# Optimization experiments

Measured on AMD Instinct MI355X. Metric: run time of the kernel, lower is better.

The kernel has to match this reference:

```python
import jax, jax.numpy as jnp
import numpy as np

B, N, D_IN, D_H, D_OUT = 32, 512, 512, 512, 512


def _xavier(key, fan_in, fan_out):
    bound = np.sqrt(6.0 / (fan_in + fan_out))
    return jax.random.uniform(key, (fan_in, fan_out), jnp.float32, -bound, bound)


def setup_inputs() -> dict:
    key = jax.random.key(0)
    ks = jax.random.split(key, 8)
    batch_graph = jax.random.normal(ks[0], (B, N, D_IN), jnp.float32)
    adj = jax.random.uniform(ks[1], (B, N, N), jnp.float32)  # per-graph adjacency blocks
    W0 = _xavier(ks[2], D_IN, D_H)
    b0 = jnp.zeros((D_H,), jnp.float32)
    W1 = _xavier(ks[3], D_H, D_H)
    b1 = jnp.zeros((D_H,), jnp.float32)
    W2 = _xavier(ks[4], D_H, D_OUT)
    b2 = jnp.zeros((D_OUT,), jnp.float32)
    return {"batch_graph": batch_graph, "adj": adj,
            "W0": W0, "b0": b0, "W1": W1, "b1": b1, "W2": W2, "b2": b2}


def _gcn_layer(h, adj, W, b):
    # GraphConvolution: adj @ (h @ W) + b, batched per graph.
    # Equivalent to big_adj @ (big_graph @ W) since big_adj is block-diagonal.
    support = jnp.einsum('bnd,de->bne', h, W)
    return jnp.einsum('bnm,bme->bne', adj, support) + b


def reference(batch_graph, adj, W0, b0, W1, b1, W2, b2):
    # dropout is identity at inference time
    h = jax.nn.relu(_gcn_layer(batch_graph, adj, W0, b0))
    h = jax.nn.relu(_gcn_layer(h, adj, W1, b1))
    h = _gcn_layer(h, adj, W2, b2)  # no activation on final layer
    return h  # [B, N, D_OUT] == torch.stack(big_graph.split(N))
```

## Files before the change

### kernel.cpp

```cpp
#include <hip/hip_runtime.h>
#include <stdint.h>

typedef __bf16 bf16x8 __attribute__((ext_vector_type(8)));
typedef float f32x4 __attribute__((ext_vector_type(4)));
typedef unsigned short u16x4 __attribute__((ext_vector_type(4)));

static __device__ __forceinline__ unsigned short f2bf(float f) {
    union { float f; unsigned u; } v; v.f = f;
    unsigned r = (v.u + 0x7FFFu + ((v.u >> 16) & 1u)) >> 16;
    return (unsigned short)r;
}

__global__ void prep_kernel(const float* __restrict__ X,
                            const float* __restrict__ adj,
                            const float* __restrict__ W0,
                            const float* __restrict__ W1,
                            const float* __restrict__ W2,
                            unsigned short* __restrict__ bufH,
                            unsigned short* __restrict__ adjB,
                            unsigned short* __restrict__ Wt) {
    const int bid = blockIdx.x;
    const int t = threadIdx.x;
    if (bid < 16384) {
        const float* src = (bid < 8192) ? X : adj;
        unsigned short* dst = (bid < 8192) ? bufH : adjB;
        const int i = (bid & 8191) * 256 + t;
        f32x4 v = ((const f32x4*)src)[i];
        u16x4 o;
        o.x = f2bf(v.x); o.y = f2bf(v.y); o.z = f2bf(v.z); o.w = f2bf(v.w);
        ((u16x4*)dst)[i] = o;
    } else {
        const int wb = bid - 16384;
        const int z = wb >> 8;
        const int tile = wb & 255;
        const float* W = (z == 0) ? W0 : (z == 1) ? W1 : W2;
        unsigned short* out = Wt + (size_t)z * (512 * 512);
        __shared__ float tileS[32][33];
        const int bx = (tile & 15) * 32, by = (tile >> 4) * 32;
        const int tx = t & 31, ty = t >> 5;
        #pragma unroll
        for (int r = 0; r < 32; r += 8)
            tileS[ty + r][tx] = W[(size_t)(by + ty + r) * 512 + (bx + tx)];
        __syncthreads();
        #pragma unroll
        for (int r = 0; r < 32; r += 8)
            out[(size_t)(bx + ty + r) * 512 + (by + tx)] = f2bf(tileS[tx][ty + r]);
    }
}

template<int LDA, int LDB, int LDO, bool BIAS, bool RELU, bool ADJ, typename OT>
__global__ __launch_bounds__(256, 2)
void gemm_abT_ct(const unsigned short* __restrict__ A,
                 const unsigned short* __restrict__ B,
                 OT* __restrict__ out, const float* __restrict__ bias,
                 long batchA, long batchB, long batchO) {
    __shared__ char SMEM[65536];
    unsigned short (*As)[8192] = (unsigned short (*)[8192])SMEM;
    unsigned short (*Bs)[8192] = (unsigned short (*)[8192])(SMEM + 32768);

    const int tid  = threadIdx.x;
    const int lane = tid & 63;
    const int wave = tid >> 6;
    const int quad = lane >> 4;
    const int l16  = lane & 15;
    const int wm   = wave & 1;
    const int wn   = wave >> 1;

    const int L = blockIdx.x;
    const int x = L & 7;
    const int j = L >> 3;
    int m0, n0;
    long z;
    if constexpr (ADJ) {
        z = x + 8 * (j >> 4);
        const int t4 = j & 15;
        m0 = (t4 & 3) * 128;
        n0 = (t4 >> 2) * 128;
    } else {
        z = 0;
        m0 = (x * 16 + (j >> 2)) * 128;
        n0 = (j & 3) * 128;
    }
    A   += (size_t)z * batchA;
    B   += (size_t)z * batchB;
    out += (size_t)z * batchO;

    const int trow8 = tid >> 3;
    const int tpos8 = (tid & 7) ^ (trow8 & 7);
    const unsigned short* aG = A + (size_t)(m0 + trow8) * LDA + tpos8 * 8;
    const unsigned short* bG = B + (size_t)(n0 + trow8) * LDB + tpos8 * 8;

    f32x4 acc[4][4];
    #pragma unroll
    for (int i = 0; i < 4; ++i)
        #pragma unroll
        for (int j2 = 0; j2 < 4; ++j2) {
            f32x4 zz = {0.f, 0.f, 0.f, 0.f};
            acc[i][j2] = zz;
        }

#define STAGE(buf, ko)                                                         \
    do {                                                                       \
        char* aL = (char*)(As[buf]) + tid * 16;                                \
        char* bL = (char*)(Bs[buf]) + tid * 16;                                \
        _Pragma("unroll")                                                      \
        for (int r = 0; r < 4; ++r)                                            \
            __builtin_amdgcn_global_load_lds(                                  \
                (__attribute__((address_space(1))) void*)(uintptr_t)(aG + (size_t)(r * 32) * LDA + (ko)), \
                (__attribute__((address_space(3))) void*)(aL + r * 4096), 16, 0, 0); \
        _Pragma("unroll")                                                      \
        for (int r = 0; r < 4; ++r)                                            \
            __builtin_amdgcn_global_load_lds(                                  \
                (__attribute__((address_space(1))) void*)(uintptr_t)(bG + (size_t)(r * 32) * LDB + (ko)), \
                (__attribute__((address_space(3))) void*)(bL + r * 4096), 16, 0, 0); \
    } while (0)

#define COMPUTE(buf)                                                           \
    do {                                                                       \
        _Pragma("unroll")                                                      \
        for (int ks = 0; ks < 2; ++ks) {                                       \
            bf16x8 af[4], bfr[4];                                              \
            _Pragma("unroll")                                                  \
            for (int i = 0; i < 4; ++i) {                                      \
                const int row = wm * 64 + i * 16 + l16;                        \
                const int idx = row * 8 + ((ks * 4 + quad) ^ (row & 7));       \
                af[i] = *(const bf16x8*)((const char*)(As[buf]) + idx * 16);   \
            }                                                                  \
            _Pragma("unroll")                                                  \
            for (int j2 = 0; j2 < 4; ++j2) {                                   \
                const int row = wn * 64 + j2 * 16 + l16;                       \
                const int idx = row * 8 + ((ks * 4 + quad) ^ (row & 7));       \
                bfr[j2] = *(const bf16x8*)((const char*)(Bs[buf]) + idx * 16); \
            }                                                                  \
            _Pragma("unroll")                                                  \
            for (int i = 0; i < 4; ++i)                                        \
                _Pragma("unroll")                                              \
                for (int j2 = 0; j2 < 4; ++j2)                                 \
                    acc[i][j2] = __builtin_amdgcn_mfma_f32_16x16x32_bf16(af[i], bfr[j2], acc[i][j2], 0, 0, 0); \
        }                                                                      \
    } while (0)

    STAGE(0, 0);
    STAGE(1, 64);

    #pragma unroll 1
    for (int kp = 0; kp < 4; ++kp) {
        const int ko = kp * 128;
        asm volatile("s_waitcnt vmcnt(8)" ::: "memory");
        __builtin_amdgcn_s_barrier();
        __builtin_amdgcn_s_setprio(1);
        COMPUTE(0);
        __builtin_amdgcn_s_setprio(0);
        asm volatile("s_waitcnt lgkmcnt(0)" ::: "memory");
        __builtin_amdgcn_sched_barrier(0);
        __builtin_amdgcn_s_barrier();
        if (kp < 3) STAGE(0, ko + 128);
        if (kp < 3) asm volatile("s_waitcnt vmcnt(8)" ::: "memory");
        else        asm volatile("s_waitcnt vmcnt(0)" ::: "memory");
        __builtin_amdgcn_s_barrier();
        __builtin_amdgcn_s_setprio(1);
        COMPUTE(1);
        __builtin_amdgcn_s_setprio(0);
        asm volatile("s_waitcnt lgkmcnt(0)" ::: "memory");
        __builtin_amdgcn_sched_barrier(0);
        __builtin_amdgcn_s_barrier();
        if (kp < 3) STAGE(1, ko + 192);
    }
#undef STAGE
#undef COMPUTE

    if constexpr (sizeof(OT) == 2) {
        unsigned short* T = (unsigned short*)SMEM;
        #pragma unroll
        for (int i = 0; i < 4; ++i) {
            const int mloc = wm * 64 + i * 16 + quad * 4;
            const int mb = m0 + mloc;
            f32x4 bb = {0.f, 0.f, 0.f, 0.f};
            if constexpr (BIAS) bb = *(const f32x4*)(bias + mb);
            const int ch  = mloc >> 3;
            const int sub = (mloc & 7) * 2;
            #pragma unroll
            for (int j2 = 0; j2 < 4; ++j2) {
                const int nloc = wn * 64 + j2 * 16 + l16;
                f32x4 v = acc[i][j2];
                if constexpr (BIAS) v += bb;
                if constexpr (RELU) {
                    v.x = v.x > 0.f ? v.x : 0.f;
                    v.y = v.y > 0.f ? v.y : 0.f;
                    v.z = v.z > 0.f ? v.z : 0.f;
                    v.w = v.w > 0.f ? v.w : 0.f;
                }
                u16x4 o;
                o.x = f2bf(v.x); o.y = f2bf(v.y); o.z = f2bf(v.z); o.w = f2bf(v.w);
                *(u16x4*)((char*)T + nloc * 256 + ((ch ^ (nloc & 7)) << 4) + sub) = o;
            }
        }
        __syncthreads();
        #pragma unroll
        for (int it = 0; it < 8; ++it) {
            const int n  = (tid >> 4) + 16 * it;
            const int cc = tid & 15;
            f32x4 d = *(const f32x4*)((const char*)T + n * 256 + ((cc ^ (n & 7)) << 4));
            *(f32x4*)((unsigned short*)out + (size_t)(n0 + n) * LDO + m0 + cc * 8) = d;
        }
    } else {
        float* T = (float*)SMEM;
        #pragma unroll
        for (int i = 0; i < 4; ++i) {
            const int mloc = wm * 64 + i * 16 + quad * 4;
            const int mb = m0 + mloc;
            f32x4 bb = {0.f, 0.f, 0.f, 0.f};
            if constexpr (BIAS) bb = *(const f32x4*)(bias + mb);
            const int ch = mloc >> 2;
            #pragma unroll
            for (int j2 = 0; j2 < 4; ++j2) {
                const int nloc = wn * 64 + j2 * 16 + l16;
                f32x4 v = acc[i][j2];
                if constexpr (BIAS) v += bb;
                if constexpr (RELU) {
                    v.x = v.x > 0.f ? v.x : 0.f;
                    v.y = v.y > 0.f ? v.y : 0.f;
                    v.z = v.z > 0.f ? v.z : 0.f;
                    v.w = v.w > 0.f ? v.w : 0.f;
                }
                *(f32x4*)((char*)T + nloc * 512 + ((ch ^ (nloc & 7)) << 4)) = v;
            }
        }
        __syncthreads();
        #pragma unroll
        for (int it = 0; it < 16; ++it) {
            const int n  = (tid >> 4) + 16 * (it >> 1);
            const int cc = (tid & 15) + 16 * (it & 1);
            f32x4 d = *(const f32x4*)((const char*)T + n * 512 + ((cc ^ (n & 7)) << 4));
            *(f32x4*)((float*)out + (size_t)(n0 + n) * LDO + m0 + cc * 4) = d;
        }
    }
}

extern "C" void kernel_launch(void* const* d_in, const int* in_sizes, int n_in,
                              void* d_out, int out_size, void* d_ws, size_t ws_size,
                              hipStream_t stream) {
    (void)in_sizes; (void)n_in; (void)out_size; (void)ws_size;
    const float* X   = (const float*)d_in[0];
    const float* adj = (const float*)d_in[1];
    const float* W0  = (const float*)d_in[2];
    const float* b0  = (const float*)d_in[3];
    const float* W1  = (const float*)d_in[4];
    const float* b1  = (const float*)d_in[5];
    const float* W2  = (const float*)d_in[6];
    const float* b2  = (const float*)d_in[7];
    float* out = (float*)d_out;

    char* ws = (char*)d_ws;
    const size_t SZ = 16777216;
    unsigned short* adjB = (unsigned short*)(ws);
    unsigned short* bufH = (unsigned short*)(ws + SZ);
    unsigned short* tmpT = (unsigned short*)(ws + 2 * SZ);
    unsigned short* Wt   = (unsigned short*)(ws + 3 * SZ);
    const unsigned short* W0t = Wt;
    const unsigned short* W1t = Wt + 262144;
    const unsigned short* W2t = Wt + 2 * 262144;

    prep_kernel<<<16384 + 768, 256, 0, stream>>>(X, adj, W0, W1, W2, bufH, adjB, Wt);

    const long BATCH = 512L * 512L;

    gemm_abT_ct<512, 512, 16384, false, false, false, unsigned short>
        <<<512, 256, 0, stream>>>(bufH, W0t, tmpT, nullptr, 0, 0, 0);
    gemm_abT_ct<16384, 512, 512, true, true, true, unsigned short>
        <<<512, 256, 0, stream>>>(tmpT, adjB, bufH, b0, 512, BATCH, BATCH);
    gemm_abT_ct<512, 512, 16384, false, false, false, unsigned short>
        <<<512, 256, 0, stream>>>(bufH, W1t, tmpT, nullptr, 0, 0, 0);
    gemm_abT_ct<16384, 512, 512, true, true, true, unsigned short>
        <<<512, 256, 0, stream>>>(tmpT, adjB, bufH, b1, 512, BATCH, BATCH);
    gemm_abT_ct<512, 512, 16384, false, false, false, unsigned short>
        <<<512, 256, 0, stream>>>(bufH, W2t, tmpT, nullptr, 0, 0, 0);
    gemm_abT_ct<16384, 512, 512, true, false, true, float>
        <<<512, 256, 0, stream>>>(tmpT, adjB, out, b2, 512, BATCH, BATCH);
}
```

Measured before the change: 195.4 us.

## Switch GEMM to 4-stage pipeline with 32-wide K tiles

Replaces the double-buffered 64-wide K staging with a four-buffer ring of 32-wide K tiles, keeping three tiles in flight while one is computed, and changes the LDS swizzle to match the 4-chunk row. The aim is deeper prefetch to hide global load latency. In exchange there are twice as many barrier and waitcnt sync points per K, each with only 16 MFMAs between them, and LDS use stays the same.

```diff
diff --git a/kernel.cpp b/kernel.cpp
--- a/kernel.cpp
+++ b/kernel.cpp
@@ -55,8 +55,6 @@
                  OT* __restrict__ out, const float* __restrict__ bias,
                  long batchA, long batchB, long batchO) {
     __shared__ char SMEM[65536];
-    unsigned short (*As)[8192] = (unsigned short (*)[8192])SMEM;
-    unsigned short (*Bs)[8192] = (unsigned short (*)[8192])(SMEM + 32768);
 
     const int tid  = threadIdx.x;
     const int lane = tid & 63;
@@ -85,10 +83,10 @@
     B   += (size_t)z * batchB;
     out += (size_t)z * batchO;
 
-    const int trow8 = tid >> 3;
-    const int tpos8 = (tid & 7) ^ (trow8 & 7);
-    const unsigned short* aG = A + (size_t)(m0 + trow8) * LDA + tpos8 * 8;
-    const unsigned short* bG = B + (size_t)(n0 + trow8) * LDB + tpos8 * 8;
+    const int trow4 = tid >> 2;
+    const int tpos4 = (tid & 3) ^ (trow4 & 3);
+    const unsigned short* aG = A + (size_t)(m0 + trow4) * LDA + tpos4 * 8;
+    const unsigned short* bG = B + (size_t)(n0 + trow4) * LDB + tpos4 * 8;
 
     f32x4 acc[4][4];
     #pragma unroll
@@ -101,73 +99,71 @@
 
 #define STAGE(buf, ko)                                                         \
     do {                                                                       \
-        char* aL = (char*)(As[buf]) + tid * 16;                                \
-        char* bL = (char*)(Bs[buf]) + tid * 16;                                \
-        _Pragma("unroll")                                                      \
-        for (int r = 0; r < 4; ++r)                                            \
+        char* aL = SMEM + (buf) * 8192 + tid * 16;                             \
+        char* bL = SMEM + 32768 + (buf) * 8192 + tid * 16;                     \
+        _Pragma("unroll")                                                      \
+        for (int r = 0; r < 2; ++r)                                            \
             __builtin_amdgcn_global_load_lds(                                  \
-                (__attribute__((address_space(1))) void*)(uintptr_t)(aG + (size_t)(r * 32) * LDA + (ko)), \
+                (__attribute__((address_space(1))) void*)(uintptr_t)(aG + (size_t)(r * 64) * LDA + (ko)), \
                 (__attribute__((address_space(3))) void*)(aL + r * 4096), 16, 0, 0); \
         _Pragma("unroll")                                                      \
-        for (int r = 0; r < 4; ++r)                                            \
+        for (int r = 0; r < 2; ++r)                                            \
             __builtin_amdgcn_global_load_lds(                                  \
-                (__attribute__((address_space(1))) void*)(uintptr_t)(bG + (size_t)(r * 32) * LDB + (ko)), \
+                (__attribute__((address_space(1))) void*)(uintptr_t)(bG + (size_t)(r * 64) * LDB + (ko)), \
                 (__attribute__((address_space(3))) void*)(bL + r * 4096), 16, 0, 0); \
     } while (0)
 
 #define COMPUTE(buf)                                                           \
     do {                                                                       \
-        _Pragma("unroll")                                                      \
-        for (int ks = 0; ks < 2; ++ks) {                                       \
-            bf16x8 af[4], bfr[4];                                              \
+        const char* Ab = SMEM + (buf) * 8192;                                  \
+        const char* Bb = SMEM + 32768 + (buf) * 8192;                          \
+        bf16x8 af[4], bfr[4];                                                  \
+        _Pragma("unroll")                                                      \
+        for (int i = 0; i < 4; ++i) {                                          \
+            const int row = wm * 64 + i * 16 + l16;                            \
+            const int idx = row * 4 + (quad ^ (row & 3));                      \
+            af[i] = *(const bf16x8*)(Ab + idx * 16);                           \
+        }                                                                      \
+        _Pragma("unroll")                                                      \
+        for (int j2 = 0; j2 < 4; ++j2) {                                       \
+            const int row = wn * 64 + j2 * 16 + l16;                           \
+            const int idx = row * 4 + (quad ^ (row & 3));                      \
+            bfr[j2] = *(const bf16x8*)(Bb + idx * 16);                         \
+        }                                                                      \
+        _Pragma("unroll")                                                      \
+        for (int i = 0; i < 4; ++i)                                            \
             _Pragma("unroll")                                                  \
-            for (int i = 0; i < 4; ++i) {                                      \
-                const int row = wm * 64 + i * 16 + l16;                        \
-                const int idx = row * 8 + ((ks * 4 + quad) ^ (row & 7));       \
-                af[i] = *(const bf16x8*)((const char*)(As[buf]) + idx * 16);   \
-            }                                                                  \
-            _Pragma("unroll")                                                  \
-            for (int j2 = 0; j2 < 4; ++j2) {                                   \
-                const int row = wn * 64 + j2 * 16 + l16;                       \
-                const int idx = row * 8 + ((ks * 4 + quad) ^ (row & 7));       \
-                bfr[j2] = *(const bf16x8*)((const char*)(Bs[buf]) + idx * 16); \
-            }                                                                  \
-            _Pragma("unroll")                                                  \
-            for (int i = 0; i < 4; ++i)                                        \
-                _Pragma("unroll")                                              \
-                for (int j2 = 0; j2 < 4; ++j2)                                 \
-                    acc[i][j2] = __builtin_amdgcn_mfma_f32_16x16x32_bf16(af[i], bfr[j2], acc[i][j2], 0, 0, 0); \
-        }                                                                      \
+            for (int j2 = 0; j2 < 4; ++j2)                                     \
+                acc[i][j2] = __builtin_amdgcn_mfma_f32_16x16x32_bf16(af[i], bfr[j2], acc[i][j2], 0, 0, 0); \
     } while (0)
 
+#define STAGE_BODY(vm, buf)                                                    \
+    do {                                                                       \
+        asm volatile("s_waitcnt vmcnt(" #vm ")" ::: "memory");                 \
+        __builtin_amdgcn_s_barrier();                                          \
+        __builtin_amdgcn_s_setprio(1);                                         \
+        COMPUTE(buf);                                                          \
+        __builtin_amdgcn_s_setprio(0);                                         \
+        asm volatile("s_waitcnt lgkmcnt(0)" ::: "memory");                     \
+        __builtin_amdgcn_sched_barrier(0);                                     \
+        __builtin_amdgcn_s_barrier();                                          \
+    } while (0)
+
     STAGE(0, 0);
-    STAGE(1, 64);
+    STAGE(1, 32);
+    STAGE(2, 64);
 
     #pragma unroll 1
-    for (int kp = 0; kp < 4; ++kp) {
-        const int ko = kp * 128;
-        asm volatile("s_waitcnt vmcnt(8)" ::: "memory");
-        __builtin_amdgcn_s_barrier();
-        __builtin_amdgcn_s_setprio(1);
-        COMPUTE(0);
-        __builtin_amdgcn_s_setprio(0);
-        asm volatile("s_waitcnt lgkmcnt(0)" ::: "memory");
-        __builtin_amdgcn_sched_barrier(0);
-        __builtin_amdgcn_s_barrier();
-        if (kp < 3) STAGE(0, ko + 128);
-        if (kp < 3) asm volatile("s_waitcnt vmcnt(8)" ::: "memory");
-        else        asm volatile("s_waitcnt vmcnt(0)" ::: "memory");
-        __builtin_amdgcn_s_barrier();
-        __builtin_amdgcn_s_setprio(1);
-        COMPUTE(1);
-        __builtin_amdgcn_s_setprio(0);
-        asm volatile("s_waitcnt lgkmcnt(0)" ::: "memory");
-        __builtin_amdgcn_sched_barrier(0);
-        __builtin_amdgcn_s_barrier();
-        if (kp < 3) STAGE(1, ko + 192);
-    }
+    for (int s = 0; s < 13; ++s) {
+        STAGE_BODY(8, s & 3);
+        STAGE((s + 3) & 3, (s + 3) * 32);
+    }
+    STAGE_BODY(8, 1);
+    STAGE_BODY(4, 2);
+    STAGE_BODY(0, 3);
 #undef STAGE
 #undef COMPUTE
+#undef STAGE_BODY
 
     if constexpr (sizeof(OT) == 2) {
         unsigned short* T = (unsigned short*)SMEM;
```

Measured after the change: 209.9 us. 7.4% more time.
